# Kernel tuning notes

Measured on AMD Instinct MI355X. Metric: run time of the kernel, lower is better.

## Reference

```python
import jax, jax.numpy as jnp
import numpy as np


def setup_inputs() -> dict:
    key = jax.random.key(0)
    k1, k2 = jax.random.split(key)
    B, N, D = 32, 4096, 768
    x = jax.random.normal(k1, (B, N + 1, D), dtype=jnp.float32)
    significance = jax.random.normal(k2, (B, N), dtype=jnp.float32)
    return {"x": x, "significance": significance, "keep_tokens": 1024}


def reference(x, significance, keep_tokens):
    # x: [B, N+1, D] with CLS at position 0; significance: [B, N]
    cls_token = x[:, :1, :]              # [B, 1, D]
    tokens = x[:, 1:, :]                 # [B, N, D]
    if keep_tokens >= tokens.shape[1]:
        return x
    # top-k significance per batch (sorted descending, matching torch.topk)
    _, topk_indices = jax.lax.top_k(significance, keep_tokens)  # [B, K]
    pooled_tokens = jnp.take_along_axis(tokens, topk_indices[:, :, None], axis=1)  # [B, K, D]
    return jnp.concatenate([cls_token, pooled_tokens], axis=1)  # [B, 1+K, D]
```

## Files before the change

### kernel.cpp

```cpp
#include <hip/hip_runtime.h>

constexpr int B    = 32;
constexpr int NTOK = 4096;
constexpr int D    = 768;
constexpr int K    = 1024;
constexpr int D4   = D / 4;
constexpr int ROWS = 5;
constexpr int GPB  = 205;

typedef float vfloat4 __attribute__((ext_vector_type(4)));

__device__ __forceinline__ unsigned monotone_u32(float f) {
  unsigned u = __float_as_uint(f);
  return (u & 0x80000000u) ? ~u : (u | 0x80000000u);
}

__device__ __forceinline__ unsigned long long mkkey(float v, unsigned gidx) {
  return ((unsigned long long)(~monotone_u32(v)) << 32) | gidx;
}

__global__ __launch_bounds__(1024)
void topk_sort(const float* __restrict__ sig, int* __restrict__ idx) {
  __shared__ unsigned long long keys[NTOK];
  const int b = blockIdx.x;
  const float* s = sig + (size_t)b * NTOK;

  #pragma unroll
  for (int rep = 0; rep < 4; ++rep) {
    int i = threadIdx.x + rep * 1024;
    keys[i] = mkkey(s[i], i);
  }
  __syncthreads();

  for (int k = 2; k <= 2048; k <<= 1) {
    for (int j = k >> 1; j > 0; j >>= 1) {
      #pragma unroll
      for (int rep = 0; rep < 2; ++rep) {
        int p = threadIdx.x + rep * 1024;
        int i = ((p & ~(j - 1)) << 1) | (p & (j - 1));
        bool dir = ((i & k) == 0);
        unsigned long long a = keys[i], d = keys[i | j];
        if ((a > d) == dir) { keys[i] = d; keys[i | j] = a; }
      }
      __syncthreads();
    }
  }

  #pragma unroll
  for (int rep = 0; rep < 2; ++rep) {
    int i = threadIdx.x + rep * 1024;
    unsigned long long a = keys[i], d = keys[i + 2048];
    if (a > d) { keys[i] = d; keys[i + 2048] = a; }
  }
  __syncthreads();
  {
    int i = threadIdx.x;
    unsigned long long a = keys[i], d = keys[i + 1024];
    if (a > d) { keys[i] = d; keys[i + 1024] = a; }
  }
  __syncthreads();
  for (int j = 512; j > 0; j >>= 1) {
    if (threadIdx.x < 512) {
      int p = threadIdx.x;
      int i = ((p & ~(j - 1)) << 1) | (p & (j - 1));
      unsigned long long a = keys[i], d = keys[i | j];
      if (a > d) { keys[i] = d; keys[i | j] = a; }
    }
    __syncthreads();
  }

  idx[b * K + threadIdx.x] = (int)(unsigned)(keys[threadIdx.x] & 0xffffffffu);
}

__global__ __launch_bounds__(D4)
void gather_kernel(const vfloat4* __restrict__ x, const int* __restrict__ idx,
                   vfloat4* __restrict__ out) {
  const int blk = blockIdx.x;
  const int b   = blk / GPB;
  const int g   = blk - b * GPB;
  const int r0  = g * ROWS;

  int src_row[ROWS];
  #pragma unroll
  for (int q = 0; q < ROWS; ++q) {
    int r = r0 + q;
    src_row[q] = (r == 0) ? 0 : 1 + idx[b * K + r - 1];
  }

  #pragma unroll
  for (int q = 0; q < ROWS; ++q) {
    int r = r0 + q;
    const size_t src = ((size_t)b * (NTOK + 1) + src_row[q]) * D4 + threadIdx.x;
    const size_t dst = ((size_t)b * (K + 1) + r) * D4 + threadIdx.x;
    vfloat4 v = __builtin_nontemporal_load(&x[src]);
    __builtin_nontemporal_store(v, &out[dst]);
  }
}

extern "C" void kernel_launch(void* const* d_in, const int* in_sizes, int n_in,
                              void* d_out, int out_size, void* d_ws, size_t ws_size,
                              hipStream_t stream) {
  const float* x   = (const float*)d_in[0];
  const float* sig = (const float*)d_in[1];
  float* out = (float*)d_out;

  int* idx = (int*)d_ws;

  topk_sort   <<<B,       1024, 0, stream>>>(sig, idx);
  gather_kernel<<<B * GPB, D4,  0, stream>>>((const vfloat4*)x, idx, (vfloat4*)out);
}
```

Baseline: 507.1 us.

## Move bitonic sort into registers with wave shuffles and flatten gather indexing

Rewrites the top-k bitonic sort so each thread holds four keys in registers. Compare-exchange steps with stride up to 32 use wave shuffles, and larger strides go through LDS, which removes most of the block-wide barriers the old shared-memory sort needed. The gather kernel becomes a flat grid-stride copy of four float4 per thread with all loads issued before the stores, and the source loads are no longer nontemporal. In exchange, every element now pays integer divides to compute its row and batch, and correctness depends on the shuffle direction logic for 64-bit keys.

```diff
diff --git a/kernel.cpp b/kernel.cpp
--- a/kernel.cpp
+++ b/kernel.cpp
@@ -1,12 +1,14 @@
 #include <hip/hip_runtime.h>
 
-constexpr int B    = 32;
-constexpr int NTOK = 4096;
-constexpr int D    = 768;
-constexpr int K    = 1024;
-constexpr int D4   = D / 4;
-constexpr int ROWS = 5;
-constexpr int GPB  = 205;
+constexpr int B     = 32;
+constexpr int NTOK  = 4096;
+constexpr int D     = 768;
+constexpr int K     = 1024;
+constexpr int D4    = D / 4;
+constexpr int NROW  = NTOK + 1;
+constexpr int OROWS = K + 1;
+constexpr int GBLK  = 6150;
+constexpr int GSTRIDE = GBLK * 256;
 
 typedef float vfloat4 __attribute__((ext_vector_type(4)));
 
@@ -19,82 +21,113 @@
   return ((unsigned long long)(~monotone_u32(v)) << 32) | gidx;
 }
 
+__device__ __forceinline__ void ce_shfl(unsigned long long& key, int e, int j, int k) {
+  unsigned long long pk = __shfl_xor(key, j);
+  bool keepMin = (((e & j) == 0) == ((e & k) == 0));
+  key = (keepMin == (key < pk)) ? key : pk;
+}
+
+__device__ __forceinline__ void ce_reg(unsigned long long& a, unsigned long long& b, bool up) {
+  unsigned long long lo = (a < b) ? a : b;
+  unsigned long long hi = (a < b) ? b : a;
+  a = up ? lo : hi;
+  b = up ? hi : lo;
+}
+
+__device__ __forceinline__ void ce_lds(unsigned long long* lds, unsigned long long key[4],
+                                       int t, int j, int k) {
+  __syncthreads();
+  #pragma unroll
+  for (int m = 0; m < 4; ++m) lds[t + m * 1024] = key[m];
+  __syncthreads();
+  #pragma unroll
+  for (int m = 0; m < 4; ++m) {
+    int e = t + m * 1024;
+    unsigned long long pk = lds[e ^ j];
+    bool keepMin = (((e & j) == 0) == ((e & k) == 0));
+    key[m] = (keepMin == (key[m] < pk)) ? key[m] : pk;
+  }
+}
+
 __global__ __launch_bounds__(1024)
 void topk_sort(const float* __restrict__ sig, int* __restrict__ idx) {
-  __shared__ unsigned long long keys[NTOK];
-  const int b = blockIdx.x;
+  __shared__ unsigned long long lds[NTOK];
+  const int b = blockIdx.x, t = threadIdx.x;
   const float* s = sig + (size_t)b * NTOK;
 
+  unsigned long long key[4];
   #pragma unroll
-  for (int rep = 0; rep < 4; ++rep) {
-    int i = threadIdx.x + rep * 1024;
-    keys[i] = mkkey(s[i], i);
+  for (int m = 0; m < 4; ++m) {
+    int e = t + m * 1024;
+    key[m] = mkkey(s[e], e);
   }
-  __syncthreads();
 
-  for (int k = 2; k <= 2048; k <<= 1) {
+  #pragma unroll
+  for (int k = 2; k <= 64; k <<= 1)
     for (int j = k >> 1; j > 0; j >>= 1) {
       #pragma unroll
-      for (int rep = 0; rep < 2; ++rep) {
-        int p = threadIdx.x + rep * 1024;
-        int i = ((p & ~(j - 1)) << 1) | (p & (j - 1));
-        bool dir = ((i & k) == 0);
-        unsigned long long a = keys[i], d = keys[i | j];
-        if ((a > d) == dir) { keys[i] = d; keys[i | j] = a; }
-      }
-      __syncthreads();
+      for (int m = 0; m < 4; ++m) ce_shfl(key[m], t + m * 1024, j, k);
+    }
+
+  for (int k = 128; k <= 512; k <<= 1) {
+    for (int j = k >> 1; j >= 64; j >>= 1) ce_lds(lds, key, t, j, k);
+    for (int j = 32; j > 0; j >>= 1) {
+      #pragma unroll
+      for (int m = 0; m < 4; ++m) ce_shfl(key[m], t + m * 1024, j, k);
     }
   }
 
-  #pragma unroll
-  for (int rep = 0; rep < 2; ++rep) {
-    int i = threadIdx.x + rep * 1024;
-    unsigned long long a = keys[i], d = keys[i + 2048];
-    if (a > d) { keys[i] = d; keys[i + 2048] = a; }
-  }
-  __syncthreads();
-  {
-    int i = threadIdx.x;
-    unsigned long long a = keys[i], d = keys[i + 1024];
-    if (a > d) { keys[i] = d; keys[i + 1024] = a; }
-  }
-  __syncthreads();
-  for (int j = 512; j > 0; j >>= 1) {
-    if (threadIdx.x < 512) {
-      int p = threadIdx.x;
-      int i = ((p & ~(j - 1)) << 1) | (p & (j - 1));
-      unsigned long long a = keys[i], d = keys[i | j];
-      if (a > d) { keys[i] = d; keys[i | j] = a; }
-    }
-    __syncthreads();
+  for (int j = 512; j >= 64; j >>= 1) ce_lds(lds, key, t, j, 1024);
+  for (int j = 32; j > 0; j >>= 1) {
+    #pragma unroll
+    for (int m = 0; m < 4; ++m) ce_shfl(key[m], t + m * 1024, j, 1024);
   }
 
-  idx[b * K + threadIdx.x] = (int)(unsigned)(keys[threadIdx.x] & 0xffffffffu);
+  ce_reg(key[0], key[1], true);
+  ce_reg(key[2], key[3], false);
+  for (int j = 512; j >= 64; j >>= 1) ce_lds(lds, key, t, j, 2048);
+  for (int j = 32; j > 0; j >>= 1) {
+    #pragma unroll
+    for (int m = 0; m < 4; ++m) ce_shfl(key[m], t + m * 1024, j, 2048);
+  }
+
+  ce_reg(key[0], key[2], true);
+  ce_reg(key[1], key[3], true);
+  ce_reg(key[0], key[1], true);
+  ce_reg(key[2], key[3], true);
+  for (int j = 512; j >= 64; j >>= 1) ce_lds(lds, key, t, j, 4096);
+  for (int j = 32; j > 0; j >>= 1) {
+    #pragma unroll
+    for (int m = 0; m < 4; ++m) ce_shfl(key[m], t + m * 1024, j, 4096);
+  }
+
+  idx[b * K + t] = (int)(unsigned)(key[0] & 0xffffffffu);
 }
 
-__global__ __launch_bounds__(D4)
+__global__ __launch_bounds__(256)
 void gather_kernel(const vfloat4* __restrict__ x, const int* __restrict__ idx,
                    vfloat4* __restrict__ out) {
-  const int blk = blockIdx.x;
-  const int b   = blk / GPB;
-  const int g   = blk - b * GPB;
-  const int r0  = g * ROWS;
+  const int tid = blockIdx.x * 256 + threadIdx.x;
 
-  int src_row[ROWS];
+  size_t src[4];
+  int    f[4];
   #pragma unroll
-  for (int q = 0; q < ROWS; ++q) {
-    int r = r0 + q;
-    src_row[q] = (r == 0) ? 0 : 1 + idx[b * K + r - 1];
+  for (int s = 0; s < 4; ++s) {
+    f[s] = tid + s * GSTRIDE;
+    int row = f[s] / D4;
+    int c   = f[s] - row * D4;
+    int bb  = row / OROWS;
+    int r   = row - bb * OROWS;
+    int src_row = 0;
+    if (r != 0) src_row = 1 + idx[bb * K + r - 1];
+    src[s] = ((size_t)bb * NROW + src_row) * D4 + c;
   }
 
+  vfloat4 v[4];
   #pragma unroll
-  for (int q = 0; q < ROWS; ++q) {
-    int r = r0 + q;
-    const size_t src = ((size_t)b * (NTOK + 1) + src_row[q]) * D4 + threadIdx.x;
-    const size_t dst = ((size_t)b * (K + 1) + r) * D4 + threadIdx.x;
-    vfloat4 v = __builtin_nontemporal_load(&x[src]);
-    __builtin_nontemporal_store(v, &out[dst]);
-  }
+  for (int s = 0; s < 4; ++s) v[s] = x[src[s]];
+  #pragma unroll
+  for (int s = 0; s < 4; ++s) __builtin_nontemporal_store(v[s], &out[f[s]]);
 }
 
 extern "C" void kernel_launch(void* const* d_in, const int* in_sizes, int n_in,
@@ -106,6 +139,6 @@
 
   int* idx = (int*)d_ws;
 
-  topk_sort   <<<B,       1024, 0, stream>>>(sig, idx);
-  gather_kernel<<<B * GPB, D4,  0, stream>>>((const vfloat4*)x, idx, (vfloat4*)out);
+  topk_sort   <<<B,    1024, 0, stream>>>(sig, idx);
+  gather_kernel<<<GBLK, 256, 0, stream>>>((const vfloat4*)x, idx, (vfloat4*)out);
 }
```

Result: slower. 518.0 us (+2.1%).
